# Performance work log

Hardware: AMD Instinct MI355X
Metric: run time of the kernel (lower is better)

Reference implementation:

```python
import jax, jax.numpy as jnp
import numpy as np
import math

B, T, E, H = 4, 2048, 1024, 16
ALPHA = 32.0


def setup_inputs() -> dict:
    key = jax.random.key(0)
    ks = jax.random.split(key, 6)
    s = 1.0 / math.sqrt(E)
    return {
        "x": jax.random.normal(ks[0], (B, T, E), dtype=jnp.float32),
        "ch_list": 0,
        "Wq": jax.random.normal(ks[1], (E, E), dtype=jnp.float32) * s,
        "bq": jnp.zeros((E,), jnp.float32),
        "Wk": jax.random.normal(ks[2], (E, E), dtype=jnp.float32) * s,
        "bk": jnp.zeros((E,), jnp.float32),
        "Wv": jax.random.normal(ks[3], (E, E), dtype=jnp.float32) * s,
        "bv": jnp.zeros((E,), jnp.float32),
        "Wp": jax.random.normal(ks[4], (E, E), dtype=jnp.float32) * s,
        "bp": jnp.zeros((E,), jnp.float32),
    }


def reference(x, ch_list, Wq, bq, Wk, bk, Wv, bv, Wp, bp):
    Bx, Tx, Ex = x.shape
    hd = Ex // H  # head dim
    # linear projections (weights stored [in, out]); split heads -> [B,H,T,hd]
    def heads(W, b):
        return (x @ W + b).reshape(Bx, Tx, H, hd).transpose(0, 2, 1, 3)
    q, k, v = heads(Wq, bq), heads(Wk, bk), heads(Wv, bv)
    scale = 1.0 / (ALPHA * math.sqrt(hd))
    qk = jnp.einsum("bhqd,bhkd->bhqk", q * scale, k)  # [B,H,T,T]
    # extra max-rescale BEFORE the causal mask (faithful to original order)
    qk = qk - jnp.max(qk, axis=-1, keepdims=True)
    causal = jnp.tril(jnp.ones((Tx, Tx), dtype=bool))  # [T,T]
    qk = jnp.where(causal[None, None], qk, -jnp.inf)
    att = jax.nn.softmax(qk * ALPHA, axis=-1)  # dropout p=0 -> identity
    y = jnp.einsum("bhqk,bhkd->bhqd", att, v)
    y = y.transpose(0, 2, 1, 3).reshape(Bx, Tx, Ex)
    return y @ Wp + bp
```

## Files before the change

kernel.cpp:

```cpp
#include <hip/hip_runtime.h>
#include <cmath>

typedef unsigned short u16;
typedef unsigned int u32;
typedef __bf16 bf16x8 __attribute__((ext_vector_type(8)));
typedef float  floatx4 __attribute__((ext_vector_type(4)));
typedef float  floatx16 __attribute__((ext_vector_type(16)));
typedef unsigned int u32x4 __attribute__((ext_vector_type(4)));

#define T_DIM 2048
#define E_DIM 1024
#define H_DIM 16
#define HD    64
#define M_DIM 8192
#define NE    8388608
#define E2    1048576
#define QSCALE 0.18033688f

__device__ __forceinline__ u16 f2bf(float f) {
    unsigned u = __builtin_bit_cast(unsigned, f);
    return (u16)((u + 0x7FFFu + ((u >> 16) & 1u)) >> 16);
}
__device__ __forceinline__ u32 pack2bf(float f0, float f1) {
    u32 a0 = __builtin_bit_cast(u32, f0) + 0x8000u;
    u32 a1 = __builtin_bit_cast(u32, f1) + 0x8000u;
    return __builtin_amdgcn_perm(a1, a0, 0x07060302u);
}

__device__ __forceinline__ void gl_lds16(const u16* g, const u16* l) {
    __builtin_amdgcn_global_load_lds(
        (const __attribute__((address_space(1))) void*)g,
        (__attribute__((address_space(3))) void*)l,
        16, 0, 0);
}

__device__ __forceinline__ bf16x8 ld_frag(const u16* p) {
    return *(const bf16x8*)p;
}

#define S_BARRIER()  asm volatile("s_barrier" ::: "memory")
#define WAIT_LGKM0() asm volatile("s_waitcnt lgkmcnt(0)" ::: "memory")

__global__ void cvt_x_kernel(const float* __restrict__ x, u16* __restrict__ xb) {
    const size_t i = (size_t)blockIdx.x * 256 + threadIdx.x;
    const float4* s = (const float4*)x + i * 2;
    const float4 a = s[0], b = s[1];
    u16 v[8] __attribute__((aligned(16)));
    v[0]=f2bf(a.x); v[1]=f2bf(a.y); v[2]=f2bf(a.z); v[3]=f2bf(a.w);
    v[4]=f2bf(b.x); v[5]=f2bf(b.y); v[6]=f2bf(b.z); v[7]=f2bf(b.w);
    *(uint4*)(xb + i * 8) = *(const uint4*)v;
}

__global__ void transpose_cvt_kernel(const float* __restrict__ w0, const float* __restrict__ w1,
                                     const float* __restrict__ w2, const float* __restrict__ w3,
                                     u16* __restrict__ out) {
    __shared__ u16 tile[64][65];
    const float* W = blockIdx.z == 0 ? w0 : blockIdx.z == 1 ? w1 : blockIdx.z == 2 ? w2 : w3;
    u16* O = out + (size_t)blockIdx.z * E2;
    const int k0 = blockIdx.y * 64, n0 = blockIdx.x * 64;
    const int r = threadIdx.x >> 2, cp = (threadIdx.x & 3) * 16;
    const float4* src = (const float4*)&W[(size_t)(k0 + r) * E_DIM + n0 + cp];
    #pragma unroll
    for (int j4 = 0; j4 < 4; ++j4) {
        const float4 f = src[j4];
        tile[r][cp + j4*4 + 0] = f2bf(f.x);
        tile[r][cp + j4*4 + 1] = f2bf(f.y);
        tile[r][cp + j4*4 + 2] = f2bf(f.z);
        tile[r][cp + j4*4 + 3] = f2bf(f.w);
    }
    __syncthreads();
    u16 vals[16] __attribute__((aligned(16)));
    #pragma unroll
    for (int j = 0; j < 16; ++j) vals[j] = tile[cp + j][r];
    u16* dst = &O[(size_t)(n0 + r) * E_DIM + k0 + cp];
    *(uint4*)dst       = *(const uint4*)vals;
    *(uint4*)(dst + 8) = *(const uint4*)(vals + 8);
}

#define NT 16

#define MFMA16(F0, N0, BQ)                                                          \
    _Pragma("unroll") for (int kk = 0; kk < 2; ++kk)                                \
    _Pragma("unroll") for (int mi = 0; mi < 4; ++mi)                                \
    _Pragma("unroll") for (int ni = 0; ni < 2; ++ni)                                \
        acc[(F0)+mi][(N0)+ni] = __builtin_amdgcn_mfma_f32_16x16x32_bf16(            \
            Aq[mi][kk], BQ[ni][kk], acc[(F0)+mi][(N0)+ni], 0, 0, 0);

template<int REMAP>
__global__ __launch_bounds__(512, 2)
void gemm256_kernel(const u16* __restrict__ A, const u16* __restrict__ Bt,
                    const float* __restrict__ bias0, const float* __restrict__ bias1,
                    const float* __restrict__ bias2, void* __restrict__ outp,
                    u16* __restrict__ vtp)
{
    __shared__ u16 SM[65536];
    const int tid = threadIdx.x;
    const int w = tid >> 6, lane = tid & 63, quad = lane >> 4, l15 = lane & 15;
    const int wm = w >> 2, wn = w & 3;

    const int nbx = (REMAP == 1) ? 12 : 4;
    const int cpx = gridDim.x >> 3;
    const int swz = ((int)blockIdx.x & 7) * cpx + ((int)blockIdx.x >> 3);
    const int bx = swz % nbx, by = swz / nbx;
    const int r0 = by * 256, c0 = bx * 256;

    const u16* pA[2]; const u16* pB[2]; unsigned lb[2];
    #pragma unroll
    for (int i = 0; i < 2; ++i) {
        const int L = i * 512 + tid, ur = L >> 3, sl = L & 7, c = sl ^ (ur & 7);
        const int ra = ((ur >> 6) << 7) + (ur & 63);
        const int nb = ((ur >> 5) << 6) + (ur & 31);
        pA[i] = A  + (size_t)(r0 + ra) * E_DIM + c * 8;
        pB[i] = Bt + (size_t)(c0 + nb) * E_DIM + c * 8;
        lb[i] = i * 8192u + (unsigned)w * 1024u;
    }
    auto stageA = [&](int kt, int u) {
        #pragma unroll
        for (int i = 0; i < 2; ++i) {
            const unsigned off = __builtin_amdgcn_readfirstlane(
                (unsigned)(kt & 1) * 32768u + (unsigned)u * 16384u + lb[i]);
            gl_lds16(pA[i] + u * (64 * E_DIM) + kt * 64,
                     (const u16*)((const char*)SM + off));
        }
    };
    auto stageB = [&](int kt, int u) {
        #pragma unroll
        for (int i = 0; i < 2; ++i) {
            const unsigned off = __builtin_amdgcn_readfirstlane(
                65536u + (unsigned)(kt & 1) * 32768u + (unsigned)u * 16384u + lb[i]);
            gl_lds16(pB[i] + u * (32 * E_DIM) + kt * 64,
                     (const u16*)((const char*)SM + off));
        }
    };

    const int arow = (wm * 64 + l15) * 64;
    const int brow = (wn * 32 + l15) * 64;
    const int sl0  = (quad ^ (l15 & 7)) * 8;

    floatx4 acc[8][4];
    #pragma unroll
    for (int f = 0; f < 8; ++f)
        #pragma unroll
        for (int n = 0; n < 4; ++n) acc[f][n] = (floatx4){0.f, 0.f, 0.f, 0.f};

    bf16x8 Aq[4][2], Bq0[2][2], Bq1[2][2];

    stageA(0, 0); stageB(0, 0); stageA(0, 1); stageB(0, 1);
    stageA(1, 0); stageB(1, 0); stageA(1, 1);
    asm volatile("s_waitcnt vmcnt(6)" ::: "memory");
    S_BARRIER();

    for (int kt = 0; kt < NT; ++kt) {
        const unsigned Ab = (unsigned)(kt & 1) * 16384u;
        const unsigned Bb = 32768u + (unsigned)(kt & 1) * 16384u;

        #pragma unroll
        for (int mi = 0; mi < 4; ++mi) {
            Aq[mi][0] = ld_frag(&SM[Ab + arow + mi * 1024 + sl0]);
            Aq[mi][1] = ld_frag(&SM[Ab + arow + mi * 1024 + (sl0 ^ 32)]);
        }
        #pragma unroll
        for (int ni = 0; ni < 2; ++ni) {
            Bq0[ni][0] = ld_frag(&SM[Bb + brow + ni * 1024 + sl0]);
            Bq0[ni][1] = ld_frag(&SM[Bb + brow + ni * 1024 + (sl0 ^ 32)]);
        }
        if (kt + 1 < NT) stageB(kt + 1, 1);
        S_BARRIER(); WAIT_LGKM0();
        __builtin_amdgcn_s_setprio(1);
        MFMA16(0, 0, Bq0)
        __builtin_amdgcn_s_setprio(0);
        S_BARRIER();

        #pragma unroll
        for (int ni = 0; ni < 2; ++ni) {
            Bq1[ni][0] = ld_frag(&SM[Bb + 8192 + brow + ni * 1024 + sl0]);
            Bq1[ni][1] = ld_frag(&SM[Bb + 8192 + brow + ni * 1024 + (sl0 ^ 32)]);
        }
        if (kt + 2 < NT) stageA(kt + 2, 0);
        S_BARRIER(); WAIT_LGKM0();
        __builtin_amdgcn_s_setprio(1);
        MFMA16(0, 2, Bq1)
        __builtin_amdgcn_s_setprio(0);
        S_BARRIER();

        #pragma unroll
        for (int mi = 0; mi < 4; ++mi) {
            Aq[mi][0] = ld_frag(&SM[Ab + 8192 + arow + mi * 1024 + sl0]);
            Aq[mi][1] = ld_frag(&SM[Ab + 8192 + arow + mi * 1024 + (sl0 ^ 32)]);
        }
        if (kt + 2 < NT) stageB(kt + 2, 0);
        S_BARRIER(); WAIT_LGKM0();
        __builtin_amdgcn_s_setprio(1);
        MFMA16(4, 2, Bq1)
        __builtin_amdgcn_s_setprio(0);
        S_BARRIER();

        if (kt + 2 < NT) stageA(kt + 2, 1);
        S_BARRIER();
        __builtin_amdgcn_s_setprio(1);
        MFMA16(4, 0, Bq0)
        __builtin_amdgcn_s_setprio(0);
        if (kt < NT - 2)       asm volatile("s_waitcnt vmcnt(6)" ::: "memory");
        else if (kt == NT - 2) asm volatile("s_waitcnt vmcnt(0)" ::: "memory");
        S_BARRIER();
    }

    #pragma unroll
    for (int n = 0; n < 4; ++n) {
        const int col = c0 + wn * 64 + n * 16 + l15;
        if (REMAP == 1) {
            const int which = col >> 10, cc = col & 1023;
            const float* bp_ = which == 0 ? bias0 : which == 1 ? bias1 : bias2;
            const float bv = bp_[cc];
            const int h = cc >> 6, d = cc & 63;
            #pragma unroll
            for (int f = 0; f < 8; ++f) {
                const int row0 = r0 + wm * 128 + f * 16 + quad * 4;
                const int b = row0 >> 11, t0 = row0 & (T_DIM - 1);
                if (which == 2) {
                    uint2 pk;
                    pk.x = pack2bf(acc[f][n][0] + bv, acc[f][n][1] + bv);
                    pk.y = pack2bf(acc[f][n][2] + bv, acc[f][n][3] + bv);
                    *(uint2*)&vtp[((size_t)((b * H_DIM + h) * HD + d)) * T_DIM + t0] = pk;
                } else {
                    #pragma unroll
                    for (int r = 0; r < 4; ++r) {
                        float val = acc[f][n][r] + bv;
                        if (which == 0) val *= QSCALE;
                        ((u16*)outp)[(size_t)which * NE +
                            (((size_t)(b * H_DIM + h) * T_DIM + (t0 + r)) * HD + d)] = f2bf(val);
                    }
                }
            }
        } else {
            const float bv = bias0[col];
            #pragma unroll
            for (int f = 0; f < 8; ++f) {
                #pragma unroll
                for (int r = 0; r < 4; ++r) {
                    const int row = r0 + wm * 128 + f * 16 + quad * 4 + r;
                    ((float*)outp)[(size_t)row * E_DIM + col] = acc[f][n][r] + bv;
                }
            }
        }
    }
}

__global__ __launch_bounds__(256, 2)
void attn_kernel(const u16* __restrict__ q, const u16* __restrict__ k,
                 const u16* __restrict__ vt, u16* __restrict__ y)
{
    __shared__ u16 Ks[2][128 * 64];
    __shared__ u16 Vs[2][64 * 128];

    const int tid = threadIdx.x;
    const int w = tid >> 6, lane = tid & 63;
    const int hl = lane >> 5, l31 = lane & 31, l7 = lane & 7;
    const int bh = blockIdx.x;
    const int qt = gridDim.y - 1 - blockIdx.y;
    const int q0 = qt * 128;
    const int b = bh >> 4, h = bh & (H_DIM - 1);
    const size_t qkb = (size_t)bh * (T_DIM * HD);
    const size_t vtb = (size_t)bh * (HD * T_DIM);

    const int qrow = q0 + w * 32 + l31;
    bf16x8 Qf[4];
    #pragma unroll
    for (int kc = 0; kc < 4; ++kc)
        Qf[kc] = ld_frag(&q[qkb + (size_t)qrow * HD + kc * 16 + hl * 8]);

    float rsum = 0.f;
    floatx16 O[2];
    #pragma unroll
    for (int i = 0; i < 16; ++i) { O[0][i] = 0.f; O[1][i] = 0.f; }

    auto stage = [&](int jt, int sel) {
        const int j0 = jt * 128;
        #pragma unroll
        for (int i = 0; i < 4; ++i) {
            const int L = i * 256 + tid;
            const unsigned off = __builtin_amdgcn_readfirstlane(i * 4096 + w * 1024);
            {   const int row = L >> 3, ch = (L & 7) ^ (row & 7);
                gl_lds16(&k[qkb + (size_t)(j0 + row) * HD + ch * 8],
                         (u16*)((char*)&Ks[sel][0] + off)); }
            {   const int row = L >> 4, ch = (L & 15) ^ (row & 7);
                gl_lds16(&vt[vtb + (size_t)row * T_DIM + j0 + ch * 8],
                         (u16*)((char*)&Vs[sel][0] + off)); }
        }
    };

    stage(0, 0);
    for (int jt = 0; jt <= qt; ++jt) {
        __syncthreads();
        if (jt < qt) stage(jt + 1, (jt + 1) & 1);
        const u16* const Kb = &Ks[jt & 1][0];
        const u16* const Vb = &Vs[jt & 1][0];

        const bool diag = (jt == qt);
        const int nkg = diag ? (w + 1) : 4;

        #pragma unroll
        for (int kg = 0; kg < 4; ++kg) {
            if (kg < nkg) {
                floatx16 S;
                #pragma unroll
                for (int i = 0; i < 16; ++i) S[i] = 0.f;
                const int krow = kg * 32 + l31;
                #pragma unroll
                for (int kc = 0; kc < 4; ++kc) {
                    const int ch = (kc * 2 + hl) ^ l7;
                    S = __builtin_amdgcn_mfma_f32_32x32x16_bf16(
                            ld_frag(&Kb[krow * 64 + ch * 8]), Qf[kc], S, 0, 0, 0);
                }

                const bool bnd = diag && (kg == w);
                u32 u[8], ru[8];
                #pragma unroll
                for (int i = 0; i < 8; ++i) {
                    const int row0 = (2*i & 3) + 8 * (i >> 1) + 4 * hl;
                    float p0 = __builtin_amdgcn_exp2f(S[2*i]);
                    float p1 = __builtin_amdgcn_exp2f(S[2*i + 1]);
                    if (bnd && (row0     > l31)) p0 = 0.f;
                    if (bnd && (row0 + 1 > l31)) p1 = 0.f;
                    rsum += p0 + p1;
                    u[i] = pack2bf(p0, p1);
                }
                #pragma unroll
                for (int i = 0; i < 8; ++i) ru[i] = __shfl_xor(u[i], 32, 64);
                const u32x4 f0 = hl ? (u32x4){ru[2], ru[3], u[2], u[3]}
                                    : (u32x4){u[0], u[1], ru[0], ru[1]};
                const u32x4 f1 = hl ? (u32x4){ru[6], ru[7], u[6], u[7]}
                                    : (u32x4){u[4], u[5], ru[4], ru[5]};

                #pragma unroll
                for (int c2 = 0; c2 < 2; ++c2) {
                    const bf16x8 Pf = __builtin_bit_cast(bf16x8, c2 ? f1 : f0);
                    const int kc16 = kg * 4 + c2 * 2 + hl;
                    #pragma unroll
                    for (int dh = 0; dh < 2; ++dh) {
                        const int d = dh * 32 + l31;
                        const int ch = kc16 ^ l7;
                        O[dh] = __builtin_amdgcn_mfma_f32_32x32x16_bf16(
                                    Pf, ld_frag(&Vb[d * 128 + ch * 8]), O[dh], 0, 0, 0);
                    }
                }
            }
        }
    }

    rsum += __shfl_xor(rsum, 32, 64);
    const float linv = 1.0f / rsum;
    #pragma unroll
    for (int i = 0; i < 16; ++i) {
        const int qr = (i & 3) + 8 * (i >> 2) + 4 * hl;
        const float lq = __shfl(linv, qr, 32);
        const int t = q0 + w * 32 + qr;
        const size_t base = ((size_t)(b * T_DIM + t)) * E_DIM + h * HD;
        y[base + l31]      = f2bf(O[0][i] * lq);
        y[base + 32 + l31] = f2bf(O[1][i] * lq);
    }
}

extern "C" void kernel_launch(void* const* d_in, const int* in_sizes, int n_in,
                              void* d_out, int out_size, void* d_ws, size_t ws_size,
                              hipStream_t stream)
{
    const float* x  = (const float*)d_in[0];
    const float* Wq = (const float*)d_in[2];
    const float* bq = (const float*)d_in[3];
    const float* Wk = (const float*)d_in[4];
    const float* bk = (const float*)d_in[5];
    const float* Wv = (const float*)d_in[6];
    const float* bv = (const float*)d_in[7];
    const float* Wp = (const float*)d_in[8];
    const float* bp = (const float*)d_in[9];

    u16* xb  = (u16*)d_ws;
    u16* wt  = xb + NE;
    u16* qb  = wt + 4 * (size_t)E2;
    u16* kb  = qb + NE;
    u16* vtb = kb + NE;
    u16* yb  = vtb + NE;

    cvt_x_kernel<<<NE / (256 * 8), 256, 0, stream>>>(x, xb);
    transpose_cvt_kernel<<<dim3(16, 16, 4), 256, 0, stream>>>(Wq, Wk, Wv, Wp, wt);
    gemm256_kernel<1><<<384, 512, 0, stream>>>(xb, wt, bq, bk, bv, qb, vtb);
    attn_kernel<<<dim3(64, 16), 256, 0, stream>>>(qb, kb, vtb, yb);
    gemm256_kernel<0><<<128, 512, 0, stream>>>(yb, wt + 3 * (size_t)E2, bp, bp, bp, (float*)d_out, nullptr);
}
```

Before: 263.7 us.

## Shrink projection GEMM tiles to 256x128 and double grid size

Result: faster. 248.0 us (-6.0%).

```diff
diff --git a/kernel.cpp b/kernel.cpp
--- a/kernel.cpp
+++ b/kernel.cpp
@@ -79,12 +79,12 @@
 
 #define NT 16
 
-#define MFMA16(F0, N0, BQ)                                                          \
-    _Pragma("unroll") for (int kk = 0; kk < 2; ++kk)                                \
-    _Pragma("unroll") for (int mi = 0; mi < 4; ++mi)                                \
-    _Pragma("unroll") for (int ni = 0; ni < 2; ++ni)                                \
-        acc[(F0)+mi][(N0)+ni] = __builtin_amdgcn_mfma_f32_16x16x32_bf16(            \
-            Aq[mi][kk], BQ[ni][kk], acc[(F0)+mi][(N0)+ni], 0, 0, 0);
+#define MFMA_Q(F0)                                                              \
+    _Pragma("unroll") for (int kk = 0; kk < 2; ++kk)                            \
+    _Pragma("unroll") for (int mi = 0; mi < 4; ++mi)                            \
+    _Pragma("unroll") for (int ni = 0; ni < 2; ++ni)                            \
+        acc[(F0)+mi][ni] = __builtin_amdgcn_mfma_f32_16x16x32_bf16(             \
+            Aq[mi][kk], Bq[ni][kk], acc[(F0)+mi][ni], 0, 0, 0);
 
 template<int REMAP>
 __global__ __launch_bounds__(512, 2)
@@ -93,26 +93,25 @@
                     const float* __restrict__ bias2, void* __restrict__ outp,
                     u16* __restrict__ vtp)
 {
-    __shared__ u16 SM[65536];
+    __shared__ u16 SM[49152];
     const int tid = threadIdx.x;
     const int w = tid >> 6, lane = tid & 63, quad = lane >> 4, l15 = lane & 15;
     const int wm = w >> 2, wn = w & 3;
 
-    const int nbx = (REMAP == 1) ? 12 : 4;
+    const int nbx = (REMAP == 1) ? 24 : 8;
     const int cpx = gridDim.x >> 3;
     const int swz = ((int)blockIdx.x & 7) * cpx + ((int)blockIdx.x >> 3);
     const int bx = swz % nbx, by = swz / nbx;
-    const int r0 = by * 256, c0 = bx * 256;
+    const int r0 = by * 256, c0 = bx * 128;
 
     const u16* pA[2]; const u16* pB[2]; unsigned lb[2];
     #pragma unroll
     for (int i = 0; i < 2; ++i) {
         const int L = i * 512 + tid, ur = L >> 3, sl = L & 7, c = sl ^ (ur & 7);
         const int ra = ((ur >> 6) << 7) + (ur & 63);
-        const int nb = ((ur >> 5) << 6) + (ur & 31);
         pA[i] = A  + (size_t)(r0 + ra) * E_DIM + c * 8;
-        pB[i] = Bt + (size_t)(c0 + nb) * E_DIM + c * 8;
-        lb[i] = i * 8192u + (unsigned)w * 1024u;
+        pB[i] = Bt + (size_t)(c0 + ur) * E_DIM + c * 8;
+        lb[i] = (unsigned)i * 8192u + (unsigned)w * 1024u;
     }
     auto stageA = [&](int kt, int u) {
         #pragma unroll
@@ -123,12 +122,12 @@
                      (const u16*)((const char*)SM + off));
         }
     };
-    auto stageB = [&](int kt, int u) {
+    auto stageB = [&](int kt) {
         #pragma unroll
         for (int i = 0; i < 2; ++i) {
             const unsigned off = __builtin_amdgcn_readfirstlane(
-                65536u + (unsigned)(kt & 1) * 32768u + (unsigned)u * 16384u + lb[i]);
-            gl_lds16(pB[i] + u * (32 * E_DIM) + kt * 64,
+                65536u + (unsigned)(kt & 1) * 16384u + lb[i]);
+            gl_lds16(pB[i] + kt * 64,
                      (const u16*)((const char*)SM + off));
         }
     };
@@ -137,22 +136,22 @@
     const int brow = (wn * 32 + l15) * 64;
     const int sl0  = (quad ^ (l15 & 7)) * 8;
 
-    floatx4 acc[8][4];
+    floatx4 acc[8][2];
     #pragma unroll
     for (int f = 0; f < 8; ++f)
         #pragma unroll
-        for (int n = 0; n < 4; ++n) acc[f][n] = (floatx4){0.f, 0.f, 0.f, 0.f};
-
-    bf16x8 Aq[4][2], Bq0[2][2], Bq1[2][2];
-
-    stageA(0, 0); stageB(0, 0); stageA(0, 1); stageB(0, 1);
-    stageA(1, 0); stageB(1, 0); stageA(1, 1);
-    asm volatile("s_waitcnt vmcnt(6)" ::: "memory");
+        for (int n = 0; n < 2; ++n) acc[f][n] = (floatx4){0.f, 0.f, 0.f, 0.f};
+
+    bf16x8 Aq[4][2], Bq[2][2];
+
+    stageA(0, 0); stageA(0, 1); stageB(0);
+    stageA(1, 0); stageB(1);
+    asm volatile("s_waitcnt vmcnt(4)" ::: "memory");
     S_BARRIER();
 
     for (int kt = 0; kt < NT; ++kt) {
         const unsigned Ab = (unsigned)(kt & 1) * 16384u;
-        const unsigned Bb = 32768u + (unsigned)(kt & 1) * 16384u;
+        const unsigned Bb = 32768u + (unsigned)(kt & 1) * 8192u;
 
         #pragma unroll
         for (int mi = 0; mi < 4; ++mi) {
@@ -161,26 +160,15 @@
         }
         #pragma unroll
         for (int ni = 0; ni < 2; ++ni) {
-            Bq0[ni][0] = ld_frag(&SM[Bb + brow + ni * 1024 + sl0]);
-            Bq0[ni][1] = ld_frag(&SM[Bb + brow + ni * 1024 + (sl0 ^ 32)]);
-        }
-        if (kt + 1 < NT) stageB(kt + 1, 1);
+            Bq[ni][0] = ld_frag(&SM[Bb + brow + ni * 1024 + sl0]);
+            Bq[ni][1] = ld_frag(&SM[Bb + brow + ni * 1024 + (sl0 ^ 32)]);
+        }
+        if (kt + 1 < NT) stageA(kt + 1, 1);
         S_BARRIER(); WAIT_LGKM0();
         __builtin_amdgcn_s_setprio(1);
-        MFMA16(0, 0, Bq0)
+        MFMA_Q(0)
         __builtin_amdgcn_s_setprio(0);
-        S_BARRIER();
-
-        #pragma unroll
-        for (int ni = 0; ni < 2; ++ni) {
-            Bq1[ni][0] = ld_frag(&SM[Bb + 8192 + brow + ni * 1024 + sl0]);
-            Bq1[ni][1] = ld_frag(&SM[Bb + 8192 + brow + ni * 1024 + (sl0 ^ 32)]);
-        }
-        if (kt + 2 < NT) stageA(kt + 2, 0);
-        S_BARRIER(); WAIT_LGKM0();
-        __builtin_amdgcn_s_setprio(1);
-        MFMA16(0, 2, Bq1)
-        __builtin_amdgcn_s_setprio(0);
+        asm volatile("s_waitcnt vmcnt(6)" ::: "memory");
         S_BARRIER();
 
         #pragma unroll
@@ -188,17 +176,10 @@
             Aq[mi][0] = ld_frag(&SM[Ab + 8192 + arow + mi * 1024 + sl0]);
             Aq[mi][1] = ld_frag(&SM[Ab + 8192 + arow + mi * 1024 + (sl0 ^ 32)]);
         }
-        if (kt + 2 < NT) stageB(kt + 2, 0);
+        if (kt + 2 < NT) { stageA(kt + 2, 0); stageB(kt + 2); }
         S_BARRIER(); WAIT_LGKM0();
         __builtin_amdgcn_s_setprio(1);
-        MFMA16(4, 2, Bq1)
-        __builtin_amdgcn_s_setprio(0);
-        S_BARRIER();
-
-        if (kt + 2 < NT) stageA(kt + 2, 1);
-        S_BARRIER();
-        __builtin_amdgcn_s_setprio(1);
-        MFMA16(4, 0, Bq0)
+        MFMA_Q(4)
         __builtin_amdgcn_s_setprio(0);
         if (kt < NT - 2)       asm volatile("s_waitcnt vmcnt(6)" ::: "memory");
         else if (kt == NT - 2) asm volatile("s_waitcnt vmcnt(0)" ::: "memory");
@@ -206,8 +187,8 @@
     }
 
     #pragma unroll
-    for (int n = 0; n < 4; ++n) {
-        const int col = c0 + wn * 64 + n * 16 + l15;
+    for (int n = 0; n < 2; ++n) {
+        const int col = c0 + wn * 32 + n * 16 + l15;
         if (REMAP == 1) {
             const int which = col >> 10, cc = col & 1023;
             const float* bp_ = which == 0 ? bias0 : which == 1 ? bias1 : bias2;
@@ -384,7 +365,7 @@
 
     cvt_x_kernel<<<NE / (256 * 8), 256, 0, stream>>>(x, xb);
     transpose_cvt_kernel<<<dim3(16, 16, 4), 256, 0, stream>>>(Wq, Wk, Wv, Wp, wt);
-    gemm256_kernel<1><<<384, 512, 0, stream>>>(xb, wt, bq, bk, bv, qb, vtb);
+    gemm256_kernel<1><<<768, 512, 0, stream>>>(xb, wt, bq, bk, bv, qb, vtb);
     attn_kernel<<<dim3(64, 16), 256, 0, stream>>>(qb, kb, vtb, yb);
-    gemm256_kernel<0><<<128, 512, 0, stream>>>(yb, wt + 3 * (size_t)E2, bp, bp, bp, (float*)d_out, nullptr);
-}
+    gemm256_kernel<0><<<256, 512, 0, stream>>>(yb, wt + 3 * (size_t)E2, bp, bp, bp, (float*)d_out, nullptr);
+}
```
